# Optimization experiments

Hardware: AMD Instinct MI355X
Metric: run time of the kernel (lower is better)

## Reference

```python
import jax, jax.numpy as jnp
import numpy as np

SIGNAL_SIZE = 33554432  # 2**25
N_ELEMENTS = 25         # log2(SIGNAL_SIZE)


def fft_shift(a, shift):
    # Faithful port of the torch fft_shift (note: 'shift' variable is reused
    # in the original; the phase ramp overwrites it after shift_samples).
    shift = 1.0 - shift
    n_samples = a.shape[-1]
    shift_samples = shift * n_samples * 0.5
    spec = jnp.fft.rfft(a, norm='ortho')
    n_coeffs = spec.shape[-1]
    phase = jnp.arange(n_coeffs) * (2j * np.pi / n_coeffs)  # complex64 ramp
    spec = spec * jnp.exp(phase * shift_samples)
    return jnp.fft.irfft(spec, n=n_samples, norm='ortho')


def setup_inputs() -> dict:
    key = jax.random.key(0)
    elements = jax.random.uniform(key, (N_ELEMENTS,), minval=-1.0, maxval=1.0,
                                  dtype=jnp.float32)
    return {"elements": elements}


def reference(elements):
    # dirac impulse of size 2 at position 0
    signal = jnp.zeros(2, dtype=jnp.float32).at[0].set(1.0)
    for i in range(N_ELEMENTS):  # fixed trip count; sizes double each step
        if i > 0:
            new_signal = jnp.zeros(signal.shape[-1] * 2, dtype=signal.dtype)
            signal = new_signal.at[::2].set(signal)
        shift_factor = 1.0 / (2 ** i)
        signal = fft_shift(signal, elements[i] * shift_factor)
    return signal  # shape [SIGNAL_SIZE]
```

## Files before the change

kernel.cpp:

```cpp
#include <hip/hip_runtime.h>


constexpr float TWOPI_F = 6.28318530717958647692f;
constexpr unsigned M24 = 1u << 24;

__device__ __forceinline__ void phase_sincos(float th, float* sn, float* cs) {
    double d = (double)th * 0.15915494309189533577;
    d -= rint(d);
    float ang = (float)(d * 6.2831853071795864769);
    __sincosf(ang, sn, cs);
}

__device__ __forceinline__ float2 cmul(float2 a, float2 f) {
    return make_float2(a.x * f.x - a.y * f.y, a.x * f.y + a.y * f.x);
}
__device__ __forceinline__ float2 caddf(float2 a, float2 b) { return make_float2(a.x + b.x, a.y + b.y); }
__device__ __forceinline__ float2 csubf(float2 a, float2 b) { return make_float2(a.x - b.x, a.y - b.y); }
__device__ __forceinline__ float2 cmulw(float2 a, float c, float s) {
    return make_float2(a.x * c - a.y * s, a.x * s + a.y * c);
}

__device__ __forceinline__ int xcd_swizzle(int b, int nblocks) {
    int chunk = nblocks >> 3;
    return (b & 7) * chunk + (b >> 3);
}

__device__ __forceinline__ void fft16_inv(float2* v) {
    const float C1 = 0.92387953251128675613f;
    const float S1 = 0.38268343236508977173f;
    const float R2 = 0.70710678118654752440f;
    float2 h[16];
#pragma unroll
    for (int b = 0; b < 4; ++b) {
        float2 s02 = caddf(v[b], v[b + 8]);
        float2 d02 = csubf(v[b], v[b + 8]);
        float2 s13 = caddf(v[b + 4], v[b + 12]);
        float2 d13 = csubf(v[b + 4], v[b + 12]);
        float2 id13 = make_float2(-d13.y, d13.x);
        h[4 * b + 0] = caddf(s02, s13);
        h[4 * b + 1] = caddf(d02, id13);
        h[4 * b + 2] = csubf(s02, s13);
        h[4 * b + 3] = csubf(d02, id13);
    }
    h[5]  = cmulw(h[5],  C1,  S1);
    h[6]  = make_float2(R2 * (h[6].x - h[6].y),  R2 * (h[6].x + h[6].y));
    h[7]  = cmulw(h[7],  S1,  C1);
    h[9]  = make_float2(R2 * (h[9].x - h[9].y),  R2 * (h[9].x + h[9].y));
    h[10] = make_float2(-h[10].y, h[10].x);
    h[11] = cmulw(h[11], -R2, R2);
    h[13] = cmulw(h[13], S1,  C1);
    h[14] = cmulw(h[14], -R2, R2);
    h[15] = cmulw(h[15], -C1, -S1);
#pragma unroll
    for (int K1 = 0; K1 < 4; ++K1) {
        float2 a = h[K1], bb = h[4 + K1], cc = h[8 + K1], dd = h[12 + K1];
        float2 sac = caddf(a, cc), dac = csubf(a, cc);
        float2 sbd = caddf(bb, dd), dbd = csubf(bb, dd);
        float2 idbd = make_float2(-dbd.y, dbd.x);
        v[K1]      = caddf(sac, sbd);
        v[K1 + 4]  = caddf(dac, idbd);
        v[K1 + 8]  = csubf(sac, sbd);
        v[K1 + 12] = csubf(dac, idbd);
    }
}

__device__ __forceinline__ void ztwiddle(float2* v, int q) {
    float ss, cc;
    __sincosf((TWOPI_F / 256.0f) * (float)q, &ss, &cc);
    float2 w = make_float2(1.0f, 0.0f), stp = make_float2(cc, ss);
#pragma unroll
    for (int K1 = 0; K1 < 16; ++K1) {
        v[K1] = cmul(v[K1], w);
        w = cmul(w, stp);
    }
}

__global__ __launch_bounds__(256) void build_q(const float* __restrict__ el,
                                               float2* __restrict__ Q) {
    __shared__ float c_s[18], s_s[18], T_s[18];
    int tid = threadIdx.x;
    if (tid < 18) {
        float e = el[tid];
        float shift1 = e * (1.0f / (float)(1u << tid));
        float sh2 = 1.0f - shift1;
        float s = sh2 * (float)(1u << tid);
        float c = (float)(6.2831853071795864769 / (double)((1u << tid) + 1u));
        c_s[tid] = c;
        s_s[tid] = s;
        float p  = (float)(1u << tid) * c;
        float th = p * s;
        float sn, cs; phase_sincos(th, &sn, &cs);
        T_s[tid] = cs;
    }
    __syncthreads();

    unsigned r = blockIdx.x * 256u + (unsigned)tid;
    if (r == 0u) { Q[0] = make_float2(1.0f, 0.0f); return; }

    unsigned t = (unsigned)__builtin_ctz(r);
    float Pr = T_s[t], Pi = 0.0f;

#pragma unroll
    for (int i = 1; i <= 17; ++i) {
        unsigned hi = 1u << i;
        int sd = (int)((r + hi) & (2u * hi - 1u)) - (int)hi;
        int K  = (i <= (int)t) ? 0 : (sd < 0 ? -sd : sd);
        float sgn = (sd < 0) ? -1.0f : 1.0f;
        float p  = (float)K * c_s[i];
        float th = p * s_s[i];
        float sn, cs; phase_sincos(th, &sn, &cs);
        float ssn = sgn * sn;
        float nr = Pr * cs - Pi * ssn;
        float ni = Pr * ssn + Pi * cs;
        Pr = nr; Pi = ni;
    }
    Q[r] = make_float2(Pr, Pi);
}

__device__ __forceinline__ float2 chain_factor(int i, unsigned k,
                                               const float* __restrict__ c_s,
                                               const float* __restrict__ s_s) {
    unsigned hi = 1u << i;
    int sd = (int)((k + hi) & (2u * hi - 1u)) - (int)hi;
    int K  = (sd < 0) ? -sd : sd;
    float sgn = (sd < 0) ? -1.0f : 1.0f;
    float p  = (float)K * c_s[i];
    float th = p * s_s[i];
    float sn, cs; phase_sincos(th, &sn, &cs);
    return make_float2(cs, sgn * sn);
}

struct WPair { float2 wk, wmk; };

__device__ __forceinline__ WPair chain_tail(unsigned k, float Pr, float Pi,
                                            const float* __restrict__ c_s,
                                            const float* __restrict__ s_s) {
    const float sc = 1.0f / 33554432.0f;
    unsigned mk = M24 - k;
    float thk = ((float)k  * c_s[24]) * s_s[24];
    float thm = ((float)mk * c_s[24]) * s_s[24];
    float snk, csk, snm, csm;
    phase_sincos(thk, &snk, &csk);
    phase_sincos(thm, &snm, &csm);

    float Skr = Pr * csk - Pi * snk;
    float Ski = Pr * snk + Pi * csk;
    float Smr = Pr * csm + Pi * snm;
    float Smi = Pr * snm - Pi * csm;

    float Ar = Skr + Smr, Ai = Ski - Smi;
    float Br = Skr - Smr, Bi = Ski + Smi;
    float ang = (float)k * (TWOPI_F / 33554432.0f);
    float ts, tc; __sincosf(ang, &ts, &tc);
    float Cr = tc * Br - ts * Bi;
    float Ci = ts * Br + tc * Bi;

    WPair w;
    w.wk  = make_float2((Ar - Ci) * sc, (Ai + Cr) * sc);
    w.wmk = make_float2((Ar + Ci) * sc, (Cr - Ai) * sc);
    return w;
}

__device__ __forceinline__ WPair chain_W(unsigned k,
                                         const float* __restrict__ c_s,
                                         const float* __restrict__ s_s,
                                         const float* __restrict__ T_s,
                                         const float2* __restrict__ Q) {
    unsigned t = (unsigned)__builtin_ctz(k);
    unsigned r = k & 0x3FFFFu;
    float Pr, Pi;
    if (r != 0u) {
        float2 q = Q[r];
        Pr = q.x; Pi = q.y;
    } else {
        Pr = T_s[t]; Pi = 0.0f;
    }
#pragma unroll
    for (int i = 18; i <= 23; ++i) {
        unsigned hi = 1u << i;
        int sd = (int)((k + hi) & (2u * hi - 1u)) - (int)hi;
        int K  = (i <= (int)t) ? 0 : (sd < 0 ? -sd : sd);
        float sgn = (sd < 0) ? -1.0f : 1.0f;
        float p  = (float)K * c_s[i];
        float th = p * s_s[i];
        float sn, cs; phase_sincos(th, &sn, &cs);
        float ssn = sgn * sn;
        float nr = Pr * cs - Pi * ssn;
        float ni = Pr * ssn + Pi * cs;
        Pr = nr; Pi = ni;
    }
    return chain_tail(k, Pr, Pi, c_s, s_s);
}

__device__ __forceinline__ int c_of_row(int b, int r) {
    if (b == 0) {
        if (r < 8)  return r;
        if (r == 8) return 32768;
        return 65536 - (r - 8);
    }
    return (r < 8) ? (8 * b + r) : (65536 - 8 * b - (r - 8));
}

__global__ __launch_bounds__(256, 3) void fused_build_fft_a(const float* __restrict__ el,
                                                            const float2* __restrict__ Q,
                                                            float2* __restrict__ out) {
    __shared__ float2 lds[16][257];
    __shared__ float c_s[25], s_s[25], T_s[24];
    int tid = threadIdx.x;
    if (tid < 25) {
        float e = el[tid];
        float shift1 = e * (1.0f / (float)(1u << tid));
        float sh2 = 1.0f - shift1;
        float s = sh2 * (float)(1u << tid);
        float c = (float)(6.2831853071795864769 / (double)((1u << tid) + 1u));
        c_s[tid] = c;
        s_s[tid] = s;
        if (tid < 24) {
            float p  = (float)(1u << tid) * c;
            float th = p * s;
            float sn, cs; phase_sincos(th, &sn, &cs);
            T_s[tid] = cs;
        }
    }
    __syncthreads();

    int b = xcd_swizzle(blockIdx.x, 4096);
    int r = tid & 15;
    int q = tid >> 4;
    int c = c_of_row(b, r);
    int rm = (b == 0 && (r == 0 || r == 8)) ? r : (r ^ 8);

    if (b == 0 && r == 0) {
#pragma unroll 1
        for (int u = 0; u < 8; ++u) {
            int k3 = q + 16 * u;
            if (k3 == 0) {
                float p  = 16777216.0f * c_s[24];
                float th = p * s_s[24];
                float sn, cs; phase_sincos(th, &sn, &cs);
                const float sc = 1.0f / 33554432.0f;
                lds[0][0] = make_float2((1.0f + cs) * sc, (1.0f - cs) * sc);
                WPair w = chain_W(8388608u, c_s, s_s, T_s, Q);
                lds[0][128] = w.wk;
            } else {
                unsigned j = (unsigned)k3 << 16;
                WPair w = chain_W(j, c_s, s_s, T_s, Q);
                lds[0][k3] = w.wk;
                lds[0][256 - k3] = w.wmk;
            }
        }
    } else {
        unsigned kbase = (unsigned)c + ((unsigned)q << 16);
        unsigned rres  = kbase & 0x3FFFFu;
        float2 P1 = Q[rres];
        P1 = cmul(P1, chain_factor(18, kbase, c_s, s_s));
        P1 = cmul(P1, chain_factor(19, kbase, c_s, s_s));
        float2 P2[2], P3[4];
#pragma unroll
        for (int j = 0; j < 2; ++j)
            P2[j] = cmul(P1, chain_factor(20, kbase + ((unsigned)j << 20), c_s, s_s));
#pragma unroll
        for (int j = 0; j < 4; ++j)
            P3[j] = cmul(P2[j & 1], chain_factor(21, kbase + ((unsigned)j << 20), c_s, s_s));

#pragma unroll 1
        for (int u = 0; u < 8; ++u) {
            int k3 = q + 16 * u;
            unsigned k = kbase + ((unsigned)u << 20);
            float2 P = cmul(P3[u & 3], chain_factor(22, k, c_s, s_s));
            P = cmul(P, chain_factor(23, k, c_s, s_s));
            WPair w = chain_tail(k, P.x, P.y, c_s, s_s);
            lds[r][k3] = w.wk;
            lds[rm][255 - k3] = w.wmk;
        }
    }
    __syncthreads();

    float2 v[16];
#pragma unroll
    for (int n1 = 0; n1 < 16; ++n1) v[n1] = lds[r][q + 16 * n1];
    fft16_inv(v);
    ztwiddle(v, q);
#pragma unroll
    for (int K1 = 0; K1 < 16; ++K1) lds[r][K1 * 16 + q] = v[K1];
    __syncthreads();

#pragma unroll
    for (int n2 = 0; n2 < 16; ++n2) v[n2] = lds[r][q * 16 + n2];
    fft16_inv(v);
#pragma unroll
    for (int K2 = 0; K2 < 16; ++K2)
        out[c + ((q + 16 * K2) << 16)] = v[K2];
}

__global__ __launch_bounds__(256, 3) void fft_stage_b(const float2* __restrict__ in,
                                                      float2* __restrict__ out) {
    __shared__ float2 lds[16][257];
    int tid = threadIdx.x;
    int wg  = xcd_swizzle(blockIdx.x, 4096);
    int k1b = (wg & 15) * 16;
    int t3  = wg >> 4;
    const float tsc = TWOPI_F / 65536.0f;
    int row = tid & 15;
    int q   = tid >> 4;

    float2 v[16];
    const float2* src = in + (k1b + row + (q << 8) + (t3 << 16));
#pragma unroll
    for (int u = 0; u < 16; ++u) v[u] = src[u << 12];

    {
        float sb, cb; __sincosf(tsc * (float)(t3 * q), &sb, &cb);
        float ssx, csx; __sincosf(tsc * (float)(t3 * 16), &ssx, &csx);
        float2 w = make_float2(cb, sb), stp = make_float2(csx, ssx);
#pragma unroll
        for (int u = 0; u < 16; ++u) {
            v[u] = cmul(v[u], w);
            w = cmul(w, stp);
        }
    }
    fft16_inv(v);
    ztwiddle(v, q);
#pragma unroll
    for (int K1 = 0; K1 < 16; ++K1) lds[row][K1 * 16 + q] = v[K1];
    __syncthreads();

#pragma unroll
    for (int n2 = 0; n2 < 16; ++n2) v[n2] = lds[row][q * 16 + n2];
    fft16_inv(v);
#pragma unroll
    for (int K2 = 0; K2 < 16; ++K2)
        out[k1b + row + ((q + 16 * K2) << 8) + (t3 << 16)] = v[K2];
}

__global__ __launch_bounds__(256, 3) void fft_stage_c(const float2* __restrict__ in,
                                                      float2* __restrict__ out) {
    __shared__ float2 lds[16][257];
    int tid = threadIdx.x;
    int wg  = xcd_swizzle(blockIdx.x, 4096);
    int t3b = (wg & 15) * 16;
    int t2  = wg >> 4;
    const float tsc = TWOPI_F / 16777216.0f;

    {
        int k1 = tid;
        const float2* src = in + (k1 + (t2 << 8) + (t3b << 16));
        float2 vb[16];
#pragma unroll
        for (int u = 0; u < 16; ++u) vb[u] = src[u << 16];
        int base = (t3b + (t2 << 8)) * k1;
        float sb, cb; __sincosf(tsc * (float)base, &sb, &cb);
        float ssx, csx; __sincosf(tsc * (float)k1, &ssx, &csx);
        float2 w = make_float2(cb, sb), stp = make_float2(csx, ssx);
#pragma unroll
        for (int u = 0; u < 16; ++u) {
            lds[u][k1] = cmul(vb[u], w);
            w = cmul(w, stp);
        }
    }
    __syncthreads();

    int rr = tid & 15;
    int q  = tid >> 4;
    float2 v[16];
#pragma unroll
    for (int n1 = 0; n1 < 16; ++n1) v[n1] = lds[rr][q + 16 * n1];
    fft16_inv(v);
    ztwiddle(v, q);
#pragma unroll
    for (int K1 = 0; K1 < 16; ++K1) lds[rr][K1 * 16 + q] = v[K1];
    __syncthreads();

#pragma unroll
    for (int n2 = 0; n2 < 16; ++n2) v[n2] = lds[rr][q * 16 + n2];
    fft16_inv(v);
#pragma unroll
    for (int K2 = 0; K2 < 16; ++K2)
        out[(t3b + rr) + (t2 << 8) + ((q + 16 * K2) << 16)] = v[K2];
}

extern "C" void kernel_launch(void* const* d_in, const int* in_sizes, int n_in,
                              void* d_out, int out_size, void* d_ws, size_t ws_size,
                              hipStream_t stream) {
    const float* el = (const float*)d_in[0];
    float2* Gd = (float2*)d_out;
    float2* Q  = (float2*)d_ws;

    hipLaunchKernelGGL(build_q,           dim3(1024), dim3(256), 0, stream, el, Q);
    hipLaunchKernelGGL(fused_build_fft_a, dim3(4096), dim3(256), 0, stream, el, Q, Gd);
    hipLaunchKernelGGL(fft_stage_b,       dim3(4096), dim3(256), 0, stream, Gd, (float2*)d_ws);
    hipLaunchKernelGGL(fft_stage_c,       dim3(4096), dim3(256), 0, stream, (float2*)d_ws, Gd);
}
```

Before: 270.9 us.

## Widen stage B/C blocks, transpose intermediate layout, swizzle LDS rows

Stage B now writes its output in a transposed order, so stage C can read contiguous 256-element rows. Stage C stages those rows through LDS with coalesced loads and applies its twiddles after reading from LDS. Both kernels move to 512-thread blocks that each handle 32 rows. The padded LDS arrays become a rotation-swizzled flat array to avoid bank conflicts. The change targets strided, uncoalesced global reads in stage C, at the cost of larger blocks, more LDS per block and an extra LDS round trip in C.

```diff
diff --git a/kernel.cpp b/kernel.cpp
--- a/kernel.cpp
+++ b/kernel.cpp
@@ -24,6 +24,8 @@
     int chunk = nblocks >> 3;
     return (b & 7) * chunk + (b >> 3);
 }
+
+#define LDSR(arr, row, col) arr[(((row) << 8) | (((col) + (row)) & 255))]
 
 __device__ __forceinline__ void fft16_inv(float2* v) {
     const float C1 = 0.92387953251128675613f;
@@ -293,16 +295,16 @@
         out[c + ((q + 16 * K2) << 16)] = v[K2];
 }
 
-__global__ __launch_bounds__(256, 3) void fft_stage_b(const float2* __restrict__ in,
+__global__ __launch_bounds__(512, 4) void fft_stage_b(const float2* __restrict__ in,
                                                       float2* __restrict__ out) {
-    __shared__ float2 lds[16][257];
+    __shared__ float2 ldsf[8192];
     int tid = threadIdx.x;
-    int wg  = xcd_swizzle(blockIdx.x, 4096);
-    int k1b = (wg & 15) * 16;
-    int t3  = wg >> 4;
+    int wg  = xcd_swizzle(blockIdx.x, 2048);
+    int k1b = (wg & 7) * 32;
+    int t3  = wg >> 3;
+    int row = tid & 31;
+    int q   = tid >> 5;
     const float tsc = TWOPI_F / 65536.0f;
-    int row = tid & 15;
-    int q   = tid >> 4;
 
     float2 v[16];
     const float2* src = in + (k1b + row + (q << 8) + (t3 << 16));
@@ -322,61 +324,61 @@
     fft16_inv(v);
     ztwiddle(v, q);
 #pragma unroll
-    for (int K1 = 0; K1 < 16; ++K1) lds[row][K1 * 16 + q] = v[K1];
-    __syncthreads();
-
-#pragma unroll
-    for (int n2 = 0; n2 < 16; ++n2) v[n2] = lds[row][q * 16 + n2];
+    for (int K1 = 0; K1 < 16; ++K1) LDSR(ldsf, row, K1 * 16 + q) = v[K1];
+    __syncthreads();
+
+#pragma unroll
+    for (int n2 = 0; n2 < 16; ++n2) v[n2] = LDSR(ldsf, row, q * 16 + n2);
     fft16_inv(v);
 #pragma unroll
     for (int K2 = 0; K2 < 16; ++K2)
-        out[k1b + row + ((q + 16 * K2) << 8) + (t3 << 16)] = v[K2];
-}
-
-__global__ __launch_bounds__(256, 3) void fft_stage_c(const float2* __restrict__ in,
+        out[((q + 16 * K2) << 16) + (t3 << 8) + (k1b + row)] = v[K2];
+}
+
+__global__ __launch_bounds__(512, 4) void fft_stage_c(const float2* __restrict__ in,
                                                       float2* __restrict__ out) {
-    __shared__ float2 lds[16][257];
+    __shared__ float2 ldsf[8192];
     int tid = threadIdx.x;
-    int wg  = xcd_swizzle(blockIdx.x, 4096);
-    int t3b = (wg & 15) * 16;
-    int t2  = wg >> 4;
+    int wg  = xcd_swizzle(blockIdx.x, 2048);
+    int t3b = (wg & 7) * 32;
+    int t2  = wg >> 3;
     const float tsc = TWOPI_F / 16777216.0f;
 
+    const float2* src = in + ((t2 << 16) + (t3b << 8));
+#pragma unroll
+    for (int i = 0; i < 16; ++i) {
+        int f = tid + 512 * i;
+        LDSR(ldsf, f >> 8, f & 255) = src[f];
+    }
+    __syncthreads();
+
+    int row = tid & 31;
+    int q   = tid >> 5;
+    int t3  = t3b + row;
+    int A   = t3 + (t2 << 8);
+    float2 v[16];
     {
-        int k1 = tid;
-        const float2* src = in + (k1 + (t2 << 8) + (t3b << 16));
-        float2 vb[16];
-#pragma unroll
-        for (int u = 0; u < 16; ++u) vb[u] = src[u << 16];
-        int base = (t3b + (t2 << 8)) * k1;
-        float sb, cb; __sincosf(tsc * (float)base, &sb, &cb);
-        float ssx, csx; __sincosf(tsc * (float)k1, &ssx, &csx);
+        float sb, cb; __sincosf(tsc * (float)(A * q), &sb, &cb);
+        float ssx, csx; __sincosf(tsc * (float)(A * 16), &ssx, &csx);
         float2 w = make_float2(cb, sb), stp = make_float2(csx, ssx);
 #pragma unroll
-        for (int u = 0; u < 16; ++u) {
-            lds[u][k1] = cmul(vb[u], w);
+        for (int n1 = 0; n1 < 16; ++n1) {
+            v[n1] = cmul(LDSR(ldsf, row, q + 16 * n1), w);
             w = cmul(w, stp);
         }
     }
-    __syncthreads();
-
-    int rr = tid & 15;
-    int q  = tid >> 4;
-    float2 v[16];
-#pragma unroll
-    for (int n1 = 0; n1 < 16; ++n1) v[n1] = lds[rr][q + 16 * n1];
     fft16_inv(v);
     ztwiddle(v, q);
 #pragma unroll
-    for (int K1 = 0; K1 < 16; ++K1) lds[rr][K1 * 16 + q] = v[K1];
-    __syncthreads();
-
-#pragma unroll
-    for (int n2 = 0; n2 < 16; ++n2) v[n2] = lds[rr][q * 16 + n2];
+    for (int K1 = 0; K1 < 16; ++K1) LDSR(ldsf, row, K1 * 16 + q) = v[K1];
+    __syncthreads();
+
+#pragma unroll
+    for (int n2 = 0; n2 < 16; ++n2) v[n2] = LDSR(ldsf, row, q * 16 + n2);
     fft16_inv(v);
 #pragma unroll
     for (int K2 = 0; K2 < 16; ++K2)
-        out[(t3b + rr) + (t2 << 8) + ((q + 16 * K2) << 16)] = v[K2];
+        out[((q + 16 * K2) << 16) + (t2 << 8) + t3] = v[K2];
 }
 
 extern "C" void kernel_launch(void* const* d_in, const int* in_sizes, int n_in,
@@ -388,6 +390,6 @@
 
     hipLaunchKernelGGL(build_q,           dim3(1024), dim3(256), 0, stream, el, Q);
     hipLaunchKernelGGL(fused_build_fft_a, dim3(4096), dim3(256), 0, stream, el, Q, Gd);
-    hipLaunchKernelGGL(fft_stage_b,       dim3(4096), dim3(256), 0, stream, Gd, (float2*)d_ws);
-    hipLaunchKernelGGL(fft_stage_c,       dim3(4096), dim3(256), 0, stream, (float2*)d_ws, Gd);
-}
+    hipLaunchKernelGGL(fft_stage_b,       dim3(2048), dim3(512), 0, stream, Gd, (float2*)d_ws);
+    hipLaunchKernelGGL(fft_stage_c,       dim3(2048), dim3(512), 0, stream, (float2*)d_ws, Gd);
+}
```

Result: slower. 277.1 us (+2.3%).
